# Optimization experiments

Measured on AMD Instinct MI355X. Metric: run time of the kernel, lower is better.

The kernel has to match this reference:

```python
import jax, jax.numpy as jnp
import numpy as np

DIM = 768
N_HEADS = 12
HEAD_DIM = DIM // N_HEADS
HIDDEN = 4 * DIM
EPS = 1e-5


def _layernorm(x, g, b):
    m = jnp.mean(x, axis=-1, keepdims=True)
    v = jnp.mean(jnp.square(x - m), axis=-1, keepdims=True)
    return (x - m) * jax.lax.rsqrt(v + EPS) * g + b


def setup_inputs() -> dict:
    key = jax.random.key(0)
    ks = jax.random.split(key, 16)
    s = lambda fan_in: 1.0 / np.sqrt(fan_in)
    return {
        "x": jax.random.normal(ks[0], (2, 2048, DIM), dtype=jnp.float32),
        "ln1_g": jnp.ones((DIM,), jnp.float32),
        "ln1_b": jnp.zeros((DIM,), jnp.float32),
        "qkv_w": jax.random.uniform(ks[1], (DIM, 3 * DIM), jnp.float32, -s(DIM), s(DIM)),
        "qkv_b": jax.random.uniform(ks[2], (3 * DIM,), jnp.float32, -s(DIM), s(DIM)),
        "proj_w": jax.random.uniform(ks[3], (DIM, DIM), jnp.float32, -s(DIM), s(DIM)),
        "proj_b": jax.random.uniform(ks[4], (DIM,), jnp.float32, -s(DIM), s(DIM)),
        "ln2_g": jnp.ones((DIM,), jnp.float32),
        "ln2_b": jnp.zeros((DIM,), jnp.float32),
        "w1": jax.random.uniform(ks[5], (DIM, HIDDEN), jnp.float32, -s(DIM), s(DIM)),
        "b1": jax.random.uniform(ks[6], (HIDDEN,), jnp.float32, -s(DIM), s(DIM)),
        "w2": jax.random.uniform(ks[7], (HIDDEN, DIM), jnp.float32, -s(HIDDEN), s(HIDDEN)),
        "b2": jax.random.uniform(ks[8], (DIM,), jnp.float32, -s(HIDDEN), s(HIDDEN)),
    }


def reference(x, ln1_g, ln1_b, qkv_w, qkv_b, proj_w, proj_b, ln2_g, ln2_b, w1, b1, w2, b2):
    B, N, C = x.shape
    # ---- attention branch (pre-norm) ----
    h = _layernorm(x, ln1_g, ln1_b)
    qkv = (h @ qkv_w + qkv_b).reshape(B, N, 3, N_HEADS, HEAD_DIM)
    qkv = qkv.transpose(2, 0, 3, 1, 4)  # [3, B, H, N, Dh]
    q, k, v = qkv[0], qkv[1], qkv[2]
    scale = HEAD_DIM ** -0.5
    scores = jnp.einsum("bhnd,bhmd->bhnm", q, k) * scale  # [B,H,N,N]
    attn = jax.nn.softmax(scores, axis=-1)
    ctx = jnp.einsum("bhnm,bhmd->bhnd", attn, v)  # [B,H,N,Dh]
    ctx = ctx.transpose(0, 2, 1, 3).reshape(B, N, C)
    x = x + ctx @ proj_w + proj_b
    # ---- MLP branch (pre-norm) ----
    h = _layernorm(x, ln2_g, ln2_b)
    h = jax.nn.gelu(h @ w1 + b1, approximate=False)  # torch nn.GELU default = exact erf
    x = x + h @ w2 + b2
    return x
```

## Files before the change

kernel.cpp:

```cpp
#include <hip/hip_runtime.h>
#include <hip/hip_bf16.h>
#include <math.h>

#define DIM 768
#define NHEADS 12
#define HDIM 64
#define HIDDEN 3072
#define SEQ 2048
#define NTOK 4096
#define QKV3 2304

typedef __attribute__((ext_vector_type(8))) __bf16 bf16x8;
typedef __attribute__((ext_vector_type(4))) float f32x4;
typedef __attribute__((ext_vector_type(16))) float f32x16;

__device__ __forceinline__ ushort f32_bf16(float f) {
  union { float f; uint u; } c{f};
  uint u = c.u;
  u = (u + 0x7FFFu + ((u >> 16) & 1u)) >> 16;
  return (ushort)u;
}

__device__ __forceinline__ float bf16_f32(ushort u) {
  union { uint u; float f; } c{(uint)u << 16};
  return c.f;
}

__device__ __forceinline__ uint cvt_pk_bf16(float lo, float hi) {
  uint r;
  asm("v_cvt_pk_bf16_f32 %0, %1, %2" : "=v"(r) : "v"(lo), "v"(hi));
  return r;
}

__device__ __forceinline__ void glds16(const ushort* g, ushort* l) {
  __builtin_amdgcn_global_load_lds(
      (const __attribute__((address_space(1))) unsigned int*)(const void*)g,
      (__attribute__((address_space(3))) unsigned int*)(void*)l, 16, 0, 0);
}

union U8 { uint u[4]; bf16x8 v; };

__global__ __launch_bounds__(256) void transpose_to_bf16(
    const float* __restrict__ in, ushort* __restrict__ out, int K, int N) {
  __shared__ float tile[32][33];
  int kb = blockIdx.y * 32, nb = blockIdx.x * 32;
  int tx = threadIdx.x, ty = threadIdx.y;
#pragma unroll
  for (int i = 0; i < 32; i += 8)
    tile[ty + i][tx] = in[(size_t)(kb + ty + i) * N + nb + tx];
  __syncthreads();
#pragma unroll
  for (int i = 0; i < 32; i += 8)
    out[(size_t)(nb + ty + i) * K + kb + tx] = f32_bf16(tile[tx][ty + i]);
}

__global__ __launch_bounds__(256) void ln_bf16(
    const float* __restrict__ x, const float* __restrict__ g,
    const float* __restrict__ bta, ushort* __restrict__ out) {
  int row = blockIdx.x;
  const float* xr = x + (size_t)row * DIM;
  int t = threadIdx.x;
  float v0 = xr[t], v1 = xr[t + 256], v2 = xr[t + 512];
  float s = v0 + v1 + v2;
  float q = v0 * v0 + v1 * v1 + v2 * v2;
#pragma unroll
  for (int m = 1; m < 64; m <<= 1) {
    s += __shfl_xor(s, m);
    q += __shfl_xor(q, m);
  }
  __shared__ float ss[4], qq[4];
  int wid = t >> 6;
  if ((t & 63) == 0) { ss[wid] = s; qq[wid] = q; }
  __syncthreads();
  s = ss[0] + ss[1] + ss[2] + ss[3];
  q = qq[0] + qq[1] + qq[2] + qq[3];
  float mean = s * (1.0f / DIM);
  float var = q * (1.0f / DIM) - mean * mean;
  float rs = rsqrtf(var + 1e-5f);
  size_t o = (size_t)row * DIM;
  out[o + t]       = f32_bf16((v0 - mean) * rs * g[t]       + bta[t]);
  out[o + t + 256] = f32_bf16((v1 - mean) * rs * g[t + 256] + bta[t + 256]);
  out[o + t + 512] = f32_bf16((v2 - mean) * rs * g[t + 512] + bta[t + 512]);
}

template <int EPI>
__global__ __launch_bounds__(256, 3) void gemm_bf16(
    const ushort* __restrict__ A, const ushort* __restrict__ Bt,
    const float* __restrict__ bias, const float* __restrict__ resid,
    void* __restrict__ outv, int M, int N, int K, int lda, int ldb,
    ushort* __restrict__ p0, ushort* __restrict__ p1, ushort* __restrict__ p2) {
  __shared__ __align__(16) ushort As[128 * 64];
  __shared__ __align__(16) ushort Bs[128 * 64];
  int t = threadIdx.x;
  int lane = t & 63, w = t >> 6;
  int wr = w >> 1, wc = w & 1;
  int m0 = blockIdx.y * 128, n0 = blockIdx.x * 128;
  int kb = blockIdx.z * K;
  f32x4 acc[4][4] = {};
  int rl = lane & 15, g = lane >> 4, rl7 = rl & 7;

  int baseRow = w * 32 + (lane >> 3);
  int cs = (lane & 7) ^ ((lane >> 3) & 7);
  const ushort* Asrc = A + (size_t)(m0 + baseRow) * lda + kb + cs * 8;
  const ushort* Bsrc = Bt + (size_t)(n0 + baseRow) * ldb + kb + cs * 8;
  ushort* Adst = &As[(w * 256 + lane) * 8];
  ushort* Bdst = &Bs[(w * 256 + lane) * 8];

  for (int k0 = 0; k0 < K; k0 += 64) {
    __syncthreads();
#pragma unroll
    for (int i = 0; i < 4; i++) {
      glds16(Asrc + (size_t)i * 8 * lda + k0, Adst + i * 512);
      glds16(Bsrc + (size_t)i * 8 * ldb + k0, Bdst + i * 512);
    }
    __syncthreads();
    bf16x8 a[2][4], b[2][4];
#pragma unroll
    for (int kk = 0; kk < 2; kk++)
#pragma unroll
      for (int i = 0; i < 4; i++) {
        a[kk][i] = *(const bf16x8*)&As[(wr * 64 + i * 16 + rl) * 64 + ((kk * 4 + g) ^ rl7) * 8];
        b[kk][i] = *(const bf16x8*)&Bs[(wc * 64 + i * 16 + rl) * 64 + ((kk * 4 + g) ^ rl7) * 8];
      }
#pragma unroll
    for (int kk = 0; kk < 2; kk++)
#pragma unroll
      for (int i = 0; i < 4; i++)
#pragma unroll
        for (int j = 0; j < 4; j++)
          acc[i][j] = __builtin_amdgcn_mfma_f32_16x16x32_bf16(a[kk][i], b[kk][j], acc[i][j], 0, 0, 0);
  }
  ushort* pz = (blockIdx.z == 0) ? p0 : ((blockIdx.z == 1) ? p1 : p2);
  int g4 = (lane >> 4) * 4;
#pragma unroll
  for (int i = 0; i < 4; i++) {
#pragma unroll
    for (int j = 0; j < 4; j++) {
      int col = n0 + wc * 64 + j * 16 + rl;
      float bval = (EPI == 3) ? 0.0f : bias[col];
#pragma unroll
      for (int r = 0; r < 4; r++) {
        int row = m0 + wr * 64 + i * 16 + g4 + r;
        float v = acc[i][j][r] + bval;
        if (EPI == 0) {
          ((ushort*)outv)[(size_t)row * N + col] = f32_bf16(v);
        } else if (EPI == 1) {
          v += resid[(size_t)row * N + col];
          ((float*)outv)[(size_t)row * N + col] = v;
        } else if (EPI == 2) {
          v = 0.5f * v * (1.0f + erff(v * 0.70710678118654752f));
          ((ushort*)outv)[(size_t)row * N + col] = f32_bf16(v);
        } else {
          pz[(size_t)row * N + col] = f32_bf16(v);
        }
      }
    }
  }
}

__global__ __launch_bounds__(256) void reduce3_kernel(
    const ushort* __restrict__ p0, const ushort* __restrict__ p1,
    const ushort* __restrict__ p2, const float* __restrict__ x1,
    const float* __restrict__ bias, float* __restrict__ out) {
  int i = blockIdx.x * 256 + threadIdx.x;
  int col = (i * 4) % DIM;
  const ushort4 a0 = ((const ushort4*)p0)[i];
  const ushort4 a1 = ((const ushort4*)p1)[i];
  const ushort4 a2 = ((const ushort4*)p2)[i];
  const float4 xv = ((const float4*)x1)[i];
  const float4 bv = *(const float4*)&bias[col];
  float4 o;
  o.x = xv.x + bv.x + bf16_f32(a0.x) + bf16_f32(a1.x) + bf16_f32(a2.x);
  o.y = xv.y + bv.y + bf16_f32(a0.y) + bf16_f32(a1.y) + bf16_f32(a2.y);
  o.z = xv.z + bv.z + bf16_f32(a0.z) + bf16_f32(a1.z) + bf16_f32(a2.z);
  o.w = xv.w + bv.w + bf16_f32(a0.w) + bf16_f32(a1.w) + bf16_f32(a2.w);
  ((float4*)out)[i] = o;
}

__global__ __launch_bounds__(256, 3) void attn_kernel(
    const ushort* __restrict__ qkv, ushort* __restrict__ ctx) {
  __shared__ __align__(16) ushort Ks[2][4096];
  __shared__ __align__(16) ushort Vt[2][4096];
  __shared__ float mml[2][2][64];
  int t = threadIdx.x, lane = t & 63, w = t >> 6;
  int qh = w & 1, kvpar = w >> 1;
  int kl = lane & 31, hi = lane >> 5;
  int qt = blockIdx.x, h = blockIdx.y, b = blockIdx.z;

  bf16x8 bq[4];
  {
    size_t qbase = (size_t)(b * SEQ + qt * 64 + qh * 32 + kl) * QKV3 + h * HDIM + hi * 8;
#pragma unroll
    for (int mi = 0; mi < 4; mi++) bq[mi] = *(const bf16x8*)(qkv + qbase + mi * 16);
  }
  f32x16 acc_o[2] = {};
  float m2 = -1e30f, lst = 0.0f;

  int pairLane = qh * 64 + lane;
  const ushort* kbase = qkv + (size_t)(b * SEQ) * QKV3 + DIM + h * HDIM;
  ushort* KsB = Ks[kvpar];
  ushort* VtB = Vt[kvpar];

  for (int it = 0; it < SEQ / 128; it++) {
    int kt = it * 2 + kvpar;
    __syncthreads();
#pragma unroll
    for (int i = 0; i < 4; i++) {
      int s = i * 128 + pairLane;
      int key = s >> 3, cc = s & 7;
      int c = cc ^ (key & 7);
      glds16(kbase + (size_t)(kt * 64 + key) * QKV3 + c * 8, &KsB[s * 8]);
    }
#pragma unroll
    for (int i = 0; i < 4; i++) {
      int s = i * 128 + pairLane;
      int key = s >> 3, c = s & 7;
      uint4 v4 = *(const uint4*)(kbase + DIM + (size_t)(kt * 64 + key) * QKV3 + c * 8);
      int co = ((key >> 3) ^ c) * 8 + (key & 7);
      uint vv[4] = {v4.x, v4.y, v4.z, v4.w};
#pragma unroll
      for (int u = 0; u < 4; u++) {
        VtB[(c * 8 + 2 * u) * 64 + co]     = (ushort)(vv[u] & 0xffffu);
        VtB[(c * 8 + 2 * u + 1) * 64 + co] = (ushort)(vv[u] >> 16);
      }
    }
    __syncthreads();

    f32x16 accs[2] = {};
    __builtin_amdgcn_s_setprio(1);
#pragma unroll
    for (int ks = 0; ks < 2; ks++) {
      int key = ks * 32 + kl;
      int kswz = key & 7;
#pragma unroll
      for (int mi = 0; mi < 4; mi++) {
        bf16x8 ak = *(const bf16x8*)&KsB[key * 64 + ((2 * mi + hi) ^ kswz) * 8];
        accs[ks] = __builtin_amdgcn_mfma_f32_32x32x16_bf16(ak, bq[mi], accs[ks], 0, 0, 0);
      }
    }
    __builtin_amdgcn_s_setprio(0);

    float mx = accs[0][0];
#pragma unroll
    for (int ks = 0; ks < 2; ks++)
#pragma unroll
      for (int r = 0; r < 16; r++) mx = fmaxf(mx, accs[ks][r]);
    mx = fmaxf(mx, __shfl_xor(mx, 32));
    float me = mx * 0.125f;
    if (!__all(me - m2 <= 8.0f)) {
      float newm = fmaxf(m2, me);
      float fac = __expf(m2 - newm);
      m2 = newm;
      lst *= fac;
#pragma unroll
      for (int r = 0; r < 16; r++) {
        int qrow = (r & 3) + 8 * (r >> 2) + 4 * hi;
        float fr = __shfl(fac, qrow | (lane & 32));
        acc_o[0][r] *= fr;
        acc_o[1][r] *= fr;
      }
    }
    float ps = 0.0f;
    uint PK[2][8];
#pragma unroll
    for (int ks = 0; ks < 2; ks++)
#pragma unroll
      for (int rp = 0; rp < 8; rp++) {
        float p0 = __expf(fmaf(accs[ks][2 * rp],     0.125f, -m2));
        float p1 = __expf(fmaf(accs[ks][2 * rp + 1], 0.125f, -m2));
        ps += p0 + p1;
        PK[ks][rp] = cvt_pk_bf16(p0, p1);
      }
    ps += __shfl_xor(ps, 32);
    lst += ps;

#pragma unroll
    for (int tt = 0; tt < 4; tt++) {
      const int ks = tt >> 1, tb = 4 * (tt & 1);
      uint e0 = hi ? PK[ks][tb]     : PK[ks][tb + 2];
      uint e1 = hi ? PK[ks][tb + 1] : PK[ks][tb + 3];
      uint x0 = __shfl_xor(e0, 32), x1 = __shfl_xor(e1, 32);
      uint l0 = hi ? PK[ks][tb + 2] : PK[ks][tb];
      uint l1 = hi ? PK[ks][tb + 3] : PK[ks][tb + 1];
      U8 a;
      a.u[0] = hi ? x0 : l0;
      a.u[1] = hi ? x1 : l1;
      a.u[2] = hi ? l0 : x0;
      a.u[3] = hi ? l1 : x1;
      __builtin_amdgcn_s_setprio(1);
#pragma unroll
      for (int dn = 0; dn < 2; dn++) {
        int d = dn * 32 + kl;
        bf16x8 bv = *(const bf16x8*)&VtB[d * 64 + ((2 * tt + hi) ^ (d >> 3)) * 8];
        acc_o[dn] = __builtin_amdgcn_mfma_f32_32x32x16_bf16(a.v, bv, acc_o[dn], 0, 0, 0);
      }
      __builtin_amdgcn_s_setprio(0);
    }
  }

  __syncthreads();
  float* obuf = (float*)(qh ? Ks[1] : Ks[0]);
  if (kvpar == 1) {
#pragma unroll
    for (int dn = 0; dn < 2; dn++)
#pragma unroll
      for (int r = 0; r < 16; r++)
        obuf[(dn * 16 + r) * 64 + lane] = acc_o[dn][r];
    mml[qh][0][lane] = m2;
    mml[qh][1][lane] = lst;
  }
  __syncthreads();
  if (kvpar == 0) {
    float mb = mml[qh][0][lane], lb = mml[qh][1][lane];
    float m = fmaxf(m2, mb);
    float fa = __expf(m2 - m), fb = __expf(mb - m);
    lst = lst * fa + lb * fb;
    float inv = 1.0f / lst;
#pragma unroll
    for (int r = 0; r < 16; r++) {
      int qrow = (r & 3) + 8 * (r >> 2) + 4 * hi;
      int src = qrow | (lane & 32);
      float far = __shfl(fa, src), fbr = __shfl(fb, src), ir = __shfl(inv, src);
      size_t row = (size_t)(b * SEQ + qt * 64 + qh * 32 + qrow);
#pragma unroll
      for (int dn = 0; dn < 2; dn++) {
        float v = (acc_o[dn][r] * far + obuf[(dn * 16 + r) * 64 + lane] * fbr) * ir;
        ctx[row * DIM + h * HDIM + dn * 32 + kl] = f32_bf16(v);
      }
    }
  }
}

extern "C" void kernel_launch(void* const* d_in, const int* in_sizes, int n_in,
                              void* d_out, int out_size, void* d_ws, size_t ws_size,
                              hipStream_t stream) {
  const float* x      = (const float*)d_in[0];
  const float* ln1_g  = (const float*)d_in[1];
  const float* ln1_b  = (const float*)d_in[2];
  const float* qkv_w  = (const float*)d_in[3];
  const float* qkv_b  = (const float*)d_in[4];
  const float* proj_w = (const float*)d_in[5];
  const float* proj_b = (const float*)d_in[6];
  const float* ln2_g  = (const float*)d_in[7];
  const float* ln2_b  = (const float*)d_in[8];
  const float* w1     = (const float*)d_in[9];
  const float* b1     = (const float*)d_in[10];
  const float* w2     = (const float*)d_in[11];
  const float* b2     = (const float*)d_in[12];
  float* out = (float*)d_out;

  char* ws = (char*)d_ws;
  size_t off = 0;
  auto alloc = [&](size_t bytes) -> void* {
    void* p = ws + off;
    off += (bytes + 255) & ~(size_t)255;
    return p;
  };
  ushort* wqkv_t  = (ushort*)alloc((size_t)QKV3 * DIM * 2);
  ushort* wproj_t = (ushort*)alloc((size_t)DIM * DIM * 2);
  ushort* w1_t    = (ushort*)alloc((size_t)HIDDEN * DIM * 2);
  ushort* w2_t    = (ushort*)alloc((size_t)DIM * HIDDEN * 2);
  ushort* hbuf    = (ushort*)alloc((size_t)NTOK * DIM * 2);
  ushort* ubuf    = (ushort*)alloc((size_t)NTOK * HIDDEN * 2);
  ushort* ctx     = (ushort*)alloc((size_t)NTOK * DIM * 2);
  float*  x1      = (float*)alloc((size_t)NTOK * DIM * 4);
  ushort* qkvbuf = ubuf;
  ushort* m1     = ubuf;
  ushort* part0 = (ushort*)ws;
  ushort* part1 = hbuf;
  ushort* part2 = ctx;

  transpose_to_bf16<<<dim3(QKV3 / 32, DIM / 32), dim3(32, 8), 0, stream>>>(qkv_w, wqkv_t, DIM, QKV3);
  transpose_to_bf16<<<dim3(DIM / 32, DIM / 32), dim3(32, 8), 0, stream>>>(proj_w, wproj_t, DIM, DIM);
  transpose_to_bf16<<<dim3(HIDDEN / 32, DIM / 32), dim3(32, 8), 0, stream>>>(w1, w1_t, DIM, HIDDEN);
  transpose_to_bf16<<<dim3(DIM / 32, HIDDEN / 32), dim3(32, 8), 0, stream>>>(w2, w2_t, HIDDEN, DIM);

  ln_bf16<<<NTOK, 256, 0, stream>>>(x, ln1_g, ln1_b, hbuf);
  gemm_bf16<0><<<dim3(QKV3 / 128, NTOK / 128), 256, 0, stream>>>(
      hbuf, wqkv_t, qkv_b, nullptr, qkvbuf, NTOK, QKV3, DIM, DIM, DIM,
      nullptr, nullptr, nullptr);
  attn_kernel<<<dim3(SEQ / 64, NHEADS, 2), 256, 0, stream>>>(qkvbuf, ctx);
  gemm_bf16<1><<<dim3(DIM / 128, NTOK / 128), 256, 0, stream>>>(
      ctx, wproj_t, proj_b, x, x1, NTOK, DIM, DIM, DIM, DIM,
      nullptr, nullptr, nullptr);
  ln_bf16<<<NTOK, 256, 0, stream>>>(x1, ln2_g, ln2_b, hbuf);
  gemm_bf16<2><<<dim3(HIDDEN / 128, NTOK / 128), 256, 0, stream>>>(
      hbuf, w1_t, b1, nullptr, m1, NTOK, HIDDEN, DIM, DIM, DIM,
      nullptr, nullptr, nullptr);
  gemm_bf16<3><<<dim3(DIM / 128, NTOK / 128, 3), 256, 0, stream>>>(
      m1, w2_t, nullptr, nullptr, nullptr, NTOK, DIM, HIDDEN / 3, HIDDEN, HIDDEN,
      part0, part1, part2);
  reduce3_kernel<<<NTOK * DIM / 4 / 256, 256, 0, stream>>>(
      part0, part1, part2, x1, b2, out);
}
```

Measured before the change: 199.1 us.

## Double-buffer K/V loads in attention and merge weight transposes into one launch

The attention kernel now double-buffers the K tile in shared memory and prefetches the next V tile into registers, so global loads for the next key block are issued before the current block's compute. This is meant to hide load latency behind the MFMA work. The four weight-transpose launches are folded into one kernel that picks its matrix from the block index, cutting launch overhead. The extra K buffer adds 16KB of shared memory per block, which may lower occupancy below the declared three blocks per CU. The hand-placed barriers and waitcnt also carry some ordering risk.

Result: faster. 192.9 us (-3.1%).

```diff
diff --git a/kernel.cpp b/kernel.cpp
--- a/kernel.cpp
+++ b/kernel.cpp
@@ -40,10 +40,20 @@
 
 union U8 { uint u[4]; bf16x8 v; };
 
-__global__ __launch_bounds__(256) void transpose_to_bf16(
-    const float* __restrict__ in, ushort* __restrict__ out, int K, int N) {
+__global__ __launch_bounds__(256) void transpose_all(
+    const float* __restrict__ qkv_w, const float* __restrict__ proj_w,
+    const float* __restrict__ w1, const float* __restrict__ w2,
+    ushort* __restrict__ o0, ushort* __restrict__ o1,
+    ushort* __restrict__ o2, ushort* __restrict__ o3) {
   __shared__ float tile[32][33];
-  int kb = blockIdx.y * 32, nb = blockIdx.x * 32;
+  int bid = blockIdx.x;
+  const float* in; ushort* out; int K, N;
+  if (bid < 1728)      { in = qkv_w;  out = o0; K = DIM;    N = QKV3; }
+  else if (bid < 2304) { bid -= 1728; in = proj_w; out = o1; K = DIM;  N = DIM; }
+  else if (bid < 4608) { bid -= 2304; in = w1;  out = o2; K = DIM;    N = HIDDEN; }
+  else                 { bid -= 4608; in = w2;  out = o3; K = HIDDEN; N = DIM; }
+  int ntx = N / 32;
+  int nb = (bid % ntx) * 32, kb = (bid / ntx) * 32;
   int tx = threadIdx.x, ty = threadIdx.y;
 #pragma unroll
   for (int i = 0; i < 32; i += 8)
@@ -179,7 +189,7 @@
 
 __global__ __launch_bounds__(256, 3) void attn_kernel(
     const ushort* __restrict__ qkv, ushort* __restrict__ ctx) {
-  __shared__ __align__(16) ushort Ks[2][4096];
+  __shared__ __align__(16) ushort Ks[2][2][4096];
   __shared__ __align__(16) ushort Vt[2][4096];
   __shared__ float mml[2][2][64];
   int t = threadIdx.x, lane = t & 63, w = t >> 6;
@@ -198,33 +208,66 @@
 
   int pairLane = qh * 64 + lane;
   const ushort* kbase = qkv + (size_t)(b * SEQ) * QKV3 + DIM + h * HDIM;
-  ushort* KsB = Ks[kvpar];
   ushort* VtB = Vt[kvpar];
 
+  int sKey[4], sCC[4];
+#pragma unroll
+  for (int i = 0; i < 4; i++) {
+    int s = i * 128 + pairLane;
+    sKey[i] = s >> 3;
+    sCC[i] = s & 7;
+  }
+
+  uint4 vpre[4];
+  {
+    int kt0 = kvpar;
+#pragma unroll
+    for (int i = 0; i < 4; i++) {
+      int c = sCC[i] ^ (sKey[i] & 7);
+      glds16(kbase + (size_t)(kt0 * 64 + sKey[i]) * QKV3 + c * 8,
+             &Ks[kvpar][0][(i * 128 + pairLane) * 8]);
+    }
+#pragma unroll
+    for (int i = 0; i < 4; i++)
+      vpre[i] = *(const uint4*)(kbase + DIM + (size_t)(kt0 * 64 + sKey[i]) * QKV3 + sCC[i] * 8);
+  }
+
   for (int it = 0; it < SEQ / 128; it++) {
-    int kt = it * 2 + kvpar;
-    __syncthreads();
+    int bufc = it & 1, bufn = bufc ^ 1;
+    int itn = (it < SEQ / 128 - 1) ? it + 1 : it;
+    int ktn = itn * 2 + kvpar;
+
+    asm volatile("" ::: "memory");
+    __builtin_amdgcn_s_barrier();
+    asm volatile("" ::: "memory");
+
 #pragma unroll
     for (int i = 0; i < 4; i++) {
-      int s = i * 128 + pairLane;
-      int key = s >> 3, cc = s & 7;
-      int c = cc ^ (key & 7);
-      glds16(kbase + (size_t)(kt * 64 + key) * QKV3 + c * 8, &KsB[s * 8]);
-    }
-#pragma unroll
-    for (int i = 0; i < 4; i++) {
-      int s = i * 128 + pairLane;
-      int key = s >> 3, c = s & 7;
-      uint4 v4 = *(const uint4*)(kbase + DIM + (size_t)(kt * 64 + key) * QKV3 + c * 8);
+      int key = sKey[i], c = sCC[i];
       int co = ((key >> 3) ^ c) * 8 + (key & 7);
-      uint vv[4] = {v4.x, v4.y, v4.z, v4.w};
+      uint vv[4] = {vpre[i].x, vpre[i].y, vpre[i].z, vpre[i].w};
 #pragma unroll
       for (int u = 0; u < 4; u++) {
         VtB[(c * 8 + 2 * u) * 64 + co]     = (ushort)(vv[u] & 0xffffu);
         VtB[(c * 8 + 2 * u + 1) * 64 + co] = (ushort)(vv[u] >> 16);
       }
     }
-    __syncthreads();
+    asm volatile("" ::: "memory");
+#pragma unroll
+    for (int i = 0; i < 4; i++) {
+      int c = sCC[i] ^ (sKey[i] & 7);
+      glds16(kbase + (size_t)(ktn * 64 + sKey[i]) * QKV3 + c * 8,
+             &Ks[kvpar][bufn][(i * 128 + pairLane) * 8]);
+    }
+#pragma unroll
+    for (int i = 0; i < 4; i++)
+      vpre[i] = *(const uint4*)(kbase + DIM + (size_t)(ktn * 64 + sKey[i]) * QKV3 + sCC[i] * 8);
+
+    asm volatile("s_waitcnt lgkmcnt(0)" ::: "memory");
+    __builtin_amdgcn_s_barrier();
+    asm volatile("" ::: "memory");
+
+    const ushort* KsB = Ks[kvpar][bufc];
 
     f32x16 accs[2] = {};
     __builtin_amdgcn_s_setprio(1);
@@ -370,10 +413,8 @@
   ushort* part1 = hbuf;
   ushort* part2 = ctx;
 
-  transpose_to_bf16<<<dim3(QKV3 / 32, DIM / 32), dim3(32, 8), 0, stream>>>(qkv_w, wqkv_t, DIM, QKV3);
-  transpose_to_bf16<<<dim3(DIM / 32, DIM / 32), dim3(32, 8), 0, stream>>>(proj_w, wproj_t, DIM, DIM);
-  transpose_to_bf16<<<dim3(HIDDEN / 32, DIM / 32), dim3(32, 8), 0, stream>>>(w1, w1_t, DIM, HIDDEN);
-  transpose_to_bf16<<<dim3(DIM / 32, HIDDEN / 32), dim3(32, 8), 0, stream>>>(w2, w2_t, HIDDEN, DIM);
+  transpose_all<<<6912, dim3(32, 8), 0, stream>>>(
+      qkv_w, proj_w, w1, w2, wqkv_t, wproj_t, w1_t, w2_t);
 
   ln_bf16<<<NTOK, 256, 0, stream>>>(x, ln1_g, ln1_b, hbuf);
   gemm_bf16<0><<<dim3(QKV3 / 128, NTOK / 128), 256, 0, stream>>>(
```
